# Kernel optimization log

Measured on AMD Instinct MI355X. Metric: run time of the kernel, lower is better.

Reference implementation:

```python
import jax, jax.numpy as jnp
import numpy as np

EPS = 1e-10

def _xavier(key, shape, gain=1.414):
    fan_in, fan_out = shape[0], shape[1]
    bound = gain * np.sqrt(6.0 / (fan_in + fan_out))
    return jax.random.uniform(key, shape, jnp.float32, -bound, bound)

def setup_inputs() -> dict:
    key = jax.random.key(0)
    ks = jax.random.split(key, 6)
    N, nfeat, nhid, nclass = 8192, 500, 64, 10
    x = jax.random.normal(ks[0], (N, nfeat), jnp.float32)
    adj = jax.random.uniform(ks[1], (N, N), jnp.float32)
    W1 = _xavier(ks[2], (nfeat, nhid))
    a1 = _xavier(ks[3], (2 * nhid, 1))
    W2 = _xavier(ks[4], (nhid, nclass))
    a2 = _xavier(ks[5], (2 * nclass, 1))
    return {"x": x, "adj": adj, "W1": W1, "a1": a1, "W2": W2, "a2": a2}

def _gat_layer(x, adj, W, a):
    # h: [N, F]
    h = x @ W
    F_out = W.shape[1]
    # e[i,j] = sigmoid(a[:F].h_i + a[F:].h_j)  (equivalent to repeat/cat/matmul)
    s_src = h @ a[:F_out, 0]   # [N]
    s_dst = h @ a[F_out:, 0]   # [N]
    e = jax.nn.sigmoid(s_src[:, None] + s_dst[None, :])  # [N, N]
    attention = e * adj
    # N != 2708/2709 -> l2 row norm branch
    norm = jnp.sqrt(jnp.sum(attention * attention, axis=1, keepdims=True)) + EPS
    attention = attention / norm
    return attention @ h

def reference(x, adj, W1, a1, W2, a2):
    h1 = _gat_layer(x, adj, W1, a1)
    # dropout is identity in eval mode
    h2 = _gat_layer(h1, adj, W2, a2)
    return jax.nn.log_softmax(h2, axis=1)
```

## Files before the change

kernel.cpp:

```cpp
#include <hip/hip_runtime.h>
#include <hip/hip_bf16.h>
#include <math.h>

typedef __attribute__((ext_vector_type(4))) float f32x4;
typedef __attribute__((ext_vector_type(4))) int   i32x4;
typedef __attribute__((ext_vector_type(8))) short short8;

#define NN 8192
#define LOG2E 1.44269504088896f

__device__ __forceinline__ unsigned f2bfu(float x) {
    unsigned u = __float_as_uint(x);
    u += 0x7FFFu + ((u >> 16) & 1u);
    return u >> 16;
}
__device__ __forceinline__ float expneg(float s) {
    return __builtin_amdgcn_exp2f(-LOG2E * s);
}

#define P1_CHUNK 100
__global__ __launch_bounds__(256) void p1_kernel(
    const float* __restrict__ x, const float* __restrict__ W1,
    const float* __restrict__ a1, float* __restrict__ h,
    float* __restrict__ fsrc, float* __restrict__ edst)
{
    __shared__ float wtile[P1_CHUNK * 64];
    const int lane = threadIdx.x & 63;
    const int w    = threadIdx.x >> 6;
    const int r0   = blockIdx.x * 8 + w * 2;

    float acc[2];
    acc[0] = 0.f; acc[1] = 0.f;

    for (int c = 0; c < 5; ++c) {
        const int kb = c * P1_CHUNK;
        __syncthreads();
        for (int idx = threadIdx.x; idx < P1_CHUNK * 64; idx += 256)
            wtile[idx] = W1[kb * 64 + idx];
        __syncthreads();
        for (int kk = 0; kk < P1_CHUNK; kk += 4) {
            float w0 = wtile[(kk + 0) * 64 + lane];
            float w1 = wtile[(kk + 1) * 64 + lane];
            float w2 = wtile[(kk + 2) * 64 + lane];
            float w3 = wtile[(kk + 3) * 64 + lane];
#pragma unroll
            for (int r = 0; r < 2; ++r) {
                f32x4 xv = *(const f32x4*)(x + (size_t)(r0 + r) * 500 + kb + kk);
                acc[r] = fmaf(xv[0], w0, acc[r]);
                acc[r] = fmaf(xv[1], w1, acc[r]);
                acc[r] = fmaf(xv[2], w2, acc[r]);
                acc[r] = fmaf(xv[3], w3, acc[r]);
            }
        }
    }
    float a_s = a1[lane], a_d = a1[64 + lane];
#pragma unroll
    for (int r = 0; r < 2; ++r) {
        h[(size_t)(r0 + r) * 64 + lane] = acc[r];
        float ps = acc[r] * a_s, pd = acc[r] * a_d;
        for (int off = 32; off > 0; off >>= 1) {
            ps += __shfl_down(ps, off); pd += __shfl_down(pd, off);
        }
        if (lane == 0) {
            fsrc[r0 + r] = expneg(ps);
            edst[r0 + r] = expneg(pd);
        }
    }
}

__global__ __launch_bounds__(256) void swizzle_kernel(
    const float* __restrict__ h, short* __restrict__ hB,
    int nblk, int ncols, int total)
{
    int tid = blockIdx.x * 256 + threadIdx.x;
    if (tid >= total) return;
    int i  = tid & 7;
    int l  = (tid >> 3) & 63;
    int t2 = tid >> 9;
    int nb = t2 % nblk;
    int kb = t2 / nblk;
    int row = kb * 32 + (l >> 4) * 8 + i;
    int col = nb * 16 + (l & 15);
    float v = h[(size_t)row * ncols + col];
    hB[tid] = (short)f2bfu(v);
}

template <int NBLK>
__global__ __launch_bounds__(1024, 8) void fused_kernel(
    const float* __restrict__ adj, const float* __restrict__ fsrc,
    const float* __restrict__ edst, const short* __restrict__ Bfrag,
    float* __restrict__ outp, float* __restrict__ normpart)
{
    __shared__ __align__(16) short Bs[16 * NBLK * 64 * 8];
    __shared__ __align__(16) float Es[512];
    const int tid  = threadIdx.x;
    const int lane = tid & 63;
    const int w    = tid >> 6;
    const int seg  = blockIdx.y;
    const int mb   = blockIdx.x * 16 + w;

    {
        const short8* src = (const short8*)(Bfrag) + (size_t)seg * (16 * NBLK * 64);
        short8* dst = (short8*)Bs;
#pragma unroll
        for (int j = 0; j < NBLK; ++j)
            dst[tid + 1024 * j] = src[tid + 1024 * j];
        if (tid < 512) Es[tid] = edst[seg * 512 + tid];
    }
    __syncthreads();

    const int r = lane >> 2;
    const int q = lane & 3;

    const float F_i = fsrc[mb * 16 + r];
    const float* arow = adj + (size_t)(mb * 16 + r) * NN + (size_t)seg * 512 + q * 4;

    const int fg = lane >> 4;
    const int fr = lane & 15;
    const int s0 = fr * 4 + (fg & 1) * 2;
    const int s1 = s0 + 1;
    const bool lowhalf = (fg < 2);

    f32x4 acc[NBLK];
#pragma unroll
    for (int nb = 0; nb < NBLK; ++nb) acc[nb] = (f32x4){0.f, 0.f, 0.f, 0.f};
    float nacc = 0.f;

    f32x4 a0c = *(const f32x4*)(arow);
    f32x4 a1c = *(const f32x4*)(arow + 16);

    for (int k = 0; k < 16; ++k) {
        f32x4 a0n, a1n;
        if (k < 15) {
            a0n = *(const f32x4*)(arow + (k + 1) * 32);
            a1n = *(const f32x4*)(arow + (k + 1) * 32 + 16);
        }
        f32x4 e0 = *(const f32x4*)&Es[k * 32 + q * 4];
        f32x4 e1 = *(const f32x4*)&Es[k * 32 + 16 + q * 4];

        float v[8];
#pragma unroll
        for (int t = 0; t < 4; ++t) {
            float sg  = __builtin_amdgcn_rcpf(fmaf(F_i, e0[t], 1.0f));
            float att = sg * a0c[t];
            nacc = fmaf(att, att, nacc);
            v[t] = att;
        }
#pragma unroll
        for (int t = 0; t < 4; ++t) {
            float sg  = __builtin_amdgcn_rcpf(fmaf(F_i, e1[t], 1.0f));
            float att = sg * a1c[t];
            nacc = fmaf(att, att, nacc);
            v[4 + t] = att;
        }
        int d0 = (int)(f2bfu(v[0]) | (f2bfu(v[1]) << 16));
        int d1 = (int)(f2bfu(v[2]) | (f2bfu(v[3]) << 16));
        int d2 = (int)(f2bfu(v[4]) | (f2bfu(v[5]) << 16));
        int d3 = (int)(f2bfu(v[6]) | (f2bfu(v[7]) << 16));

        int p00 = __shfl(d0, s0, 64), p01 = __shfl(d1, s0, 64);
        int p10 = __shfl(d0, s1, 64), p11 = __shfl(d1, s1, 64);
        int q00 = __shfl(d2, s0, 64), q01 = __shfl(d3, s0, 64);
        int q10 = __shfl(d2, s1, 64), q11 = __shfl(d3, s1, 64);
        i32x4 wv;
        wv[0] = lowhalf ? p00 : q00;
        wv[1] = lowhalf ? p01 : q01;
        wv[2] = lowhalf ? p10 : q10;
        wv[3] = lowhalf ? p11 : q11;
        short8 af = *(short8*)&wv;

#pragma unroll
        for (int nb = 0; nb < NBLK; ++nb) {
            short8 bf = *(const short8*)&Bs[((k * NBLK + nb) * 64 + lane) * 8];
            acc[nb] = __builtin_amdgcn_mfma_f32_16x16x32_bf16(af, bf, acc[nb], 0, 0, 0);
        }
        a0c = a0n; a1c = a1n;
    }

    nacc += __shfl_xor(nacc, 1);
    nacc += __shfl_xor(nacc, 2);
    if (q == 0) normpart[(mb * 16 + r) * 16 + seg] = nacc;

    constexpr int F = NBLK * 16;
#pragma unroll
    for (int nb = 0; nb < NBLK; ++nb)
#pragma unroll
        for (int rr = 0; rr < 4; ++rr)
            outp[((size_t)seg * NN + mb * 16 + fg * 4 + rr) * F + nb * 16 + fr]
                = acc[nb][rr];
}

__global__ __launch_bounds__(256) void r1_kernel(
    const float* __restrict__ outp, const float* __restrict__ normpart,
    float* __restrict__ h1)
{
    int tid = blockIdx.x * 256 + threadIdx.x;
    int i = tid >> 6, f = tid & 63;
    float s = 0.f;
#pragma unroll
    for (int sg = 0; sg < 16; ++sg)
        s += outp[((size_t)sg * NN + i) * 64 + f];
    float n = 0.f;
#pragma unroll
    for (int p = 0; p < 16; ++p) n += normpart[i * 16 + p];
    h1[tid] = s / (sqrtf(n) + 1e-10f);
}

__global__ __launch_bounds__(256) void p2_kernel(
    const float* __restrict__ h1, const float* __restrict__ W2,
    const float* __restrict__ a2, float* __restrict__ z,
    float* __restrict__ fsrc2, float* __restrict__ edst2)
{
    int i = blockIdx.x * 256 + threadIdx.x;
    if (i >= NN) return;
    float zz[10];
#pragma unroll
    for (int c = 0; c < 10; ++c) zz[c] = 0.f;
    for (int f = 0; f < 64; ++f) {
        float hv = h1[(size_t)i * 64 + f];
#pragma unroll
        for (int c = 0; c < 10; ++c) zz[c] = fmaf(hv, W2[f * 10 + c], zz[c]);
    }
    float s1 = 0.f, s2 = 0.f;
#pragma unroll
    for (int c = 0; c < 10; ++c) {
        s1 = fmaf(zz[c], a2[c], s1);
        s2 = fmaf(zz[c], a2[10 + c], s2);
        z[(size_t)i * 16 + c] = zz[c];
    }
#pragma unroll
    for (int c = 10; c < 16; ++c) z[(size_t)i * 16 + c] = 0.f;
    fsrc2[i] = expneg(s1);
    edst2[i] = expneg(s2);
}

__global__ __launch_bounds__(256) void r2_kernel(
    const float* __restrict__ outp, const float* __restrict__ normpart,
    float* __restrict__ out)
{
    int i = blockIdx.x * 256 + threadIdx.x;
    if (i >= NN) return;
    float n = 0.f;
#pragma unroll
    for (int p = 0; p < 16; ++p) n += normpart[i * 16 + p];
    float inv = 1.0f / (sqrtf(n) + 1e-10f);
    float v[10];
    float m = -1e30f;
#pragma unroll
    for (int c = 0; c < 10; ++c) {
        float s = 0.f;
#pragma unroll
        for (int sg = 0; sg < 16; ++sg)
            s += outp[((size_t)sg * NN + i) * 16 + c];
        v[c] = s * inv;
        m = fmaxf(m, v[c]);
    }
    float es = 0.f;
#pragma unroll
    for (int c = 0; c < 10; ++c) es += expf(v[c] - m);
    float lse = m + logf(es);
#pragma unroll
    for (int c = 0; c < 10; ++c) out[(size_t)i * 10 + c] = v[c] - lse;
}

extern "C" void kernel_launch(void* const* d_in, const int* in_sizes, int n_in,
                              void* d_out, int out_size, void* d_ws, size_t ws_size,
                              hipStream_t stream)
{
    const float* x   = (const float*)d_in[0];
    const float* adj = (const float*)d_in[1];
    const float* W1  = (const float*)d_in[2];
    const float* a1  = (const float*)d_in[3];
    const float* W2  = (const float*)d_in[4];
    const float* a2  = (const float*)d_in[5];
    float* out = (float*)d_out;

    char* ws = (char*)d_ws;
    size_t off = 0;
    auto alloc = [&](size_t bytes) -> void* {
        void* p = ws + off;
        off += (bytes + 255) & ~(size_t)255;
        return p;
    };
    float* h      = (float*)alloc((size_t)NN * 64 * 4);
    float* fsrc1  = (float*)alloc((size_t)NN * 4);
    float* edst1  = (float*)alloc((size_t)NN * 4);
    short* hB1    = (short*)alloc((size_t)NN * 64 * 2);
    float* outp1  = (float*)alloc((size_t)16 * NN * 64 * 4);
    float* normp1 = (float*)alloc((size_t)NN * 16 * 4);
    float* h1     = (float*)alloc((size_t)NN * 64 * 4);
    float* z      = (float*)alloc((size_t)NN * 16 * 4);
    float* fsrc2  = (float*)alloc((size_t)NN * 4);
    float* edst2  = (float*)alloc((size_t)NN * 4);
    short* zB     = (short*)alloc((size_t)NN * 16 * 2);
    float* outp2  = (float*)alloc((size_t)16 * NN * 16 * 4);
    float* normp2 = (float*)alloc((size_t)NN * 16 * 4);

    hipLaunchKernelGGL(p1_kernel, dim3(NN / 8), dim3(256), 0, stream,
                       x, W1, a1, h, fsrc1, edst1);
    hipLaunchKernelGGL(swizzle_kernel, dim3(2048), dim3(256), 0, stream,
                       h, hB1, 4, 64, NN * 64);
    hipLaunchKernelGGL((fused_kernel<4>), dim3(32, 16), dim3(1024), 0, stream,
                       adj, fsrc1, edst1, hB1, outp1, normp1);
    hipLaunchKernelGGL(r1_kernel, dim3(2048), dim3(256), 0, stream,
                       outp1, normp1, h1);
    hipLaunchKernelGGL(p2_kernel, dim3(32), dim3(256), 0, stream,
                       h1, W2, a2, z, fsrc2, edst2);
    hipLaunchKernelGGL(swizzle_kernel, dim3(512), dim3(256), 0, stream,
                       z, zB, 1, 16, NN * 16);
    hipLaunchKernelGGL((fused_kernel<1>), dim3(32, 16), dim3(1024), 0, stream,
                       adj, fsrc2, edst2, zB, outp2, normp2);
    hipLaunchKernelGGL(r2_kernel, dim3(32), dim3(256), 0, stream,
                       outp2, normp2, out);
}
```

Before: 186.8 us.

## Process two row tiles per wave in fused kernel and fuse z swizzle into p2

Each wave in the fused attention kernel now handles two 16-row M tiles instead of one. Blocks shrink to 512 threads, and every B fragment read from LDS feeds two MFMAs, which doubles the loads in flight per wave. Separately, p2 writes the bf16 swizzled z fragments directly, removing the second swizzle launch and the fp32 z buffer. The cost is higher register pressure (twice the accumulators and prefetch registers) and fewer waves per block.

```diff
diff --git a/kernel.cpp b/kernel.cpp
--- a/kernel.cpp
+++ b/kernel.cpp
@@ -86,7 +86,7 @@
 }
 
 template <int NBLK>
-__global__ __launch_bounds__(1024, 8) void fused_kernel(
+__global__ __launch_bounds__(512, 4) void fused_kernel(
     const float* __restrict__ adj, const float* __restrict__ fsrc,
     const float* __restrict__ edst, const short* __restrict__ Bfrag,
     float* __restrict__ outp, float* __restrict__ normpart)
@@ -97,23 +97,25 @@
     const int lane = tid & 63;
     const int w    = tid >> 6;
     const int seg  = blockIdx.y;
-    const int mb   = blockIdx.x * 16 + w;
+    const int mb0  = blockIdx.x * 16 + w * 2;
 
     {
         const short8* src = (const short8*)(Bfrag) + (size_t)seg * (16 * NBLK * 64);
         short8* dst = (short8*)Bs;
 #pragma unroll
-        for (int j = 0; j < NBLK; ++j)
-            dst[tid + 1024 * j] = src[tid + 1024 * j];
-        if (tid < 512) Es[tid] = edst[seg * 512 + tid];
+        for (int j = 0; j < 2 * NBLK; ++j)
+            dst[tid + 512 * j] = src[tid + 512 * j];
+        Es[tid] = edst[seg * 512 + tid];
     }
     __syncthreads();
 
     const int r = lane >> 2;
     const int q = lane & 3;
 
-    const float F_i = fsrc[mb * 16 + r];
-    const float* arow = adj + (size_t)(mb * 16 + r) * NN + (size_t)seg * 512 + q * 4;
+    const float F0 = fsrc[mb0 * 16 + r];
+    const float F1 = fsrc[mb0 * 16 + 16 + r];
+    const float* ar0 = adj + (size_t)(mb0 * 16 + r) * NN + (size_t)seg * 512 + q * 4;
+    const float* ar1 = ar0 + (size_t)16 * NN;
 
     const int fg = lane >> 4;
     const int fr = lane & 15;
@@ -121,35 +123,27 @@
     const int s1 = s0 + 1;
     const bool lowhalf = (fg < 2);
 
-    f32x4 acc[NBLK];
-#pragma unroll
-    for (int nb = 0; nb < NBLK; ++nb) acc[nb] = (f32x4){0.f, 0.f, 0.f, 0.f};
-    float nacc = 0.f;
-
-    f32x4 a0c = *(const f32x4*)(arow);
-    f32x4 a1c = *(const f32x4*)(arow + 16);
-
-    for (int k = 0; k < 16; ++k) {
-        f32x4 a0n, a1n;
-        if (k < 15) {
-            a0n = *(const f32x4*)(arow + (k + 1) * 32);
-            a1n = *(const f32x4*)(arow + (k + 1) * 32 + 16);
-        }
-        f32x4 e0 = *(const f32x4*)&Es[k * 32 + q * 4];
-        f32x4 e1 = *(const f32x4*)&Es[k * 32 + 16 + q * 4];
-
+    f32x4 acc[2][NBLK];
+#pragma unroll
+    for (int m = 0; m < 2; ++m)
+#pragma unroll
+        for (int nb = 0; nb < NBLK; ++nb) acc[m][nb] = (f32x4){0.f, 0.f, 0.f, 0.f};
+    float nacc0 = 0.f, nacc1 = 0.f;
+
+    auto mkfrag = [&](f32x4 a0, f32x4 a1, f32x4 e0, f32x4 e1, float F_i,
+                      float& nacc) -> short8 {
         float v[8];
 #pragma unroll
         for (int t = 0; t < 4; ++t) {
             float sg  = __builtin_amdgcn_rcpf(fmaf(F_i, e0[t], 1.0f));
-            float att = sg * a0c[t];
+            float att = sg * a0[t];
             nacc = fmaf(att, att, nacc);
             v[t] = att;
         }
 #pragma unroll
         for (int t = 0; t < 4; ++t) {
             float sg  = __builtin_amdgcn_rcpf(fmaf(F_i, e1[t], 1.0f));
-            float att = sg * a1c[t];
+            float att = sg * a1[t];
             nacc = fmaf(att, att, nacc);
             v[4 + t] = att;
         }
@@ -157,7 +151,6 @@
         int d1 = (int)(f2bfu(v[2]) | (f2bfu(v[3]) << 16));
         int d2 = (int)(f2bfu(v[4]) | (f2bfu(v[5]) << 16));
         int d3 = (int)(f2bfu(v[6]) | (f2bfu(v[7]) << 16));
-
         int p00 = __shfl(d0, s0, 64), p01 = __shfl(d1, s0, 64);
         int p10 = __shfl(d0, s1, 64), p11 = __shfl(d1, s1, 64);
         int q00 = __shfl(d2, s0, 64), q01 = __shfl(d3, s0, 64);
@@ -167,27 +160,55 @@
         wv[1] = lowhalf ? p01 : q01;
         wv[2] = lowhalf ? p10 : q10;
         wv[3] = lowhalf ? p11 : q11;
-        short8 af = *(short8*)&wv;
+        return *(short8*)&wv;
+    };
+
+    f32x4 c00 = *(const f32x4*)(ar0);
+    f32x4 c01 = *(const f32x4*)(ar0 + 16);
+    f32x4 c10 = *(const f32x4*)(ar1);
+    f32x4 c11 = *(const f32x4*)(ar1 + 16);
+
+    for (int k = 0; k < 16; ++k) {
+        f32x4 n00, n01, n10, n11;
+        if (k < 15) {
+            n00 = *(const f32x4*)(ar0 + (k + 1) * 32);
+            n01 = *(const f32x4*)(ar0 + (k + 1) * 32 + 16);
+            n10 = *(const f32x4*)(ar1 + (k + 1) * 32);
+            n11 = *(const f32x4*)(ar1 + (k + 1) * 32 + 16);
+        }
+        f32x4 e0 = *(const f32x4*)&Es[k * 32 + q * 4];
+        f32x4 e1 = *(const f32x4*)&Es[k * 32 + 16 + q * 4];
+
+        short8 af0 = mkfrag(c00, c01, e0, e1, F0, nacc0);
+        short8 af1 = mkfrag(c10, c11, e0, e1, F1, nacc1);
 
 #pragma unroll
         for (int nb = 0; nb < NBLK; ++nb) {
             short8 bf = *(const short8*)&Bs[((k * NBLK + nb) * 64 + lane) * 8];
-            acc[nb] = __builtin_amdgcn_mfma_f32_16x16x32_bf16(af, bf, acc[nb], 0, 0, 0);
-        }
-        a0c = a0n; a1c = a1n;
-    }
-
-    nacc += __shfl_xor(nacc, 1);
-    nacc += __shfl_xor(nacc, 2);
-    if (q == 0) normpart[(mb * 16 + r) * 16 + seg] = nacc;
+            acc[0][nb] = __builtin_amdgcn_mfma_f32_16x16x32_bf16(af0, bf, acc[0][nb], 0, 0, 0);
+            acc[1][nb] = __builtin_amdgcn_mfma_f32_16x16x32_bf16(af1, bf, acc[1][nb], 0, 0, 0);
+        }
+        c00 = n00; c01 = n01; c10 = n10; c11 = n11;
+    }
+
+    nacc0 += __shfl_xor(nacc0, 1);
+    nacc0 += __shfl_xor(nacc0, 2);
+    nacc1 += __shfl_xor(nacc1, 1);
+    nacc1 += __shfl_xor(nacc1, 2);
+    if (q == 0) {
+        normpart[(mb0 * 16 + r) * 16 + seg]      = nacc0;
+        normpart[(mb0 * 16 + 16 + r) * 16 + seg] = nacc1;
+    }
 
     constexpr int F = NBLK * 16;
 #pragma unroll
-    for (int nb = 0; nb < NBLK; ++nb)
-#pragma unroll
-        for (int rr = 0; rr < 4; ++rr)
-            outp[((size_t)seg * NN + mb * 16 + fg * 4 + rr) * F + nb * 16 + fr]
-                = acc[nb][rr];
+    for (int m = 0; m < 2; ++m)
+#pragma unroll
+        for (int nb = 0; nb < NBLK; ++nb)
+#pragma unroll
+            for (int rr = 0; rr < 4; ++rr)
+                outp[((size_t)seg * NN + mb0 * 16 + m * 16 + fg * 4 + rr) * F
+                     + nb * 16 + fr] = acc[m][nb][rr];
 }
 
 __global__ __launch_bounds__(256) void r1_kernel(
@@ -208,7 +229,7 @@
 
 __global__ __launch_bounds__(256) void p2_kernel(
     const float* __restrict__ h1, const float* __restrict__ W2,
-    const float* __restrict__ a2, float* __restrict__ z,
+    const float* __restrict__ a2, short* __restrict__ zB,
     float* __restrict__ fsrc2, float* __restrict__ edst2)
 {
     int i = blockIdx.x * 256 + threadIdx.x;
@@ -222,14 +243,19 @@
         for (int c = 0; c < 10; ++c) zz[c] = fmaf(hv, W2[f * 10 + c], zz[c]);
     }
     float s1 = 0.f, s2 = 0.f;
+    const int kb   = i >> 5;
+    const int rowk = i & 31;
+    const int lhi  = (rowk >> 3) << 4;
+    const int j    = rowk & 7;
 #pragma unroll
     for (int c = 0; c < 10; ++c) {
         s1 = fmaf(zz[c], a2[c], s1);
         s2 = fmaf(zz[c], a2[10 + c], s2);
-        z[(size_t)i * 16 + c] = zz[c];
-    }
-#pragma unroll
-    for (int c = 10; c < 16; ++c) z[(size_t)i * 16 + c] = 0.f;
+        zB[((size_t)kb * 64 + (lhi | c)) * 8 + j] = (short)f2bfu(zz[c]);
+    }
+#pragma unroll
+    for (int c = 10; c < 16; ++c)
+        zB[((size_t)kb * 64 + (lhi | c)) * 8 + j] = 0;
     fsrc2[i] = expneg(s1);
     edst2[i] = expneg(s2);
 }
@@ -289,7 +315,6 @@
     float* outp1  = (float*)alloc((size_t)16 * NN * 64 * 4);
     float* normp1 = (float*)alloc((size_t)NN * 16 * 4);
     float* h1     = (float*)alloc((size_t)NN * 64 * 4);
-    float* z      = (float*)alloc((size_t)NN * 16 * 4);
     float* fsrc2  = (float*)alloc((size_t)NN * 4);
     float* edst2  = (float*)alloc((size_t)NN * 4);
     short* zB     = (short*)alloc((size_t)NN * 16 * 2);
@@ -300,15 +325,13 @@
                        x, W1, a1, h, fsrc1, edst1);
     hipLaunchKernelGGL(swizzle_kernel, dim3(2048), dim3(256), 0, stream,
                        h, hB1, 4, 64, NN * 64);
-    hipLaunchKernelGGL((fused_kernel<4>), dim3(32, 16), dim3(1024), 0, stream,
+    hipLaunchKernelGGL((fused_kernel<4>), dim3(32, 16), dim3(512), 0, stream,
                        adj, fsrc1, edst1, hB1, outp1, normp1);
     hipLaunchKernelGGL(r1_kernel, dim3(2048), dim3(256), 0, stream,
                        outp1, normp1, h1);
     hipLaunchKernelGGL(p2_kernel, dim3(32), dim3(256), 0, stream,
-                       h1, W2, a2, z, fsrc2, edst2);
-    hipLaunchKernelGGL(swizzle_kernel, dim3(512), dim3(256), 0, stream,
-                       z, zB, 1, 16, NN * 16);
-    hipLaunchKernelGGL((fused_kernel<1>), dim3(32, 16), dim3(1024), 0, stream,
+                       h1, W2, a2, zB, fsrc2, edst2);
+    hipLaunchKernelGGL((fused_kernel<1>), dim3(32, 16), dim3(512), 0, stream,
                        adj, fsrc2, edst2, zB, outp2, normp2);
     hipLaunchKernelGGL(r2_kernel, dim3(32), dim3(256), 0, stream,
                        outp2, normp2, out);
```

Result: faster. 179.4 us (-3.9%).
